# Performance work log

Measured on AMD Instinct MI355X. Metric: run time of the kernel, lower is better.

Reference implementation:

```python
import jax, jax.numpy as jnp
import numpy as np

B, T, D, U = 64, 1024, 300, 300


def setup_inputs() -> dict:
    key = jax.random.key(0)
    ks = jax.random.split(key, 12)
    inputs = jax.random.normal(ks[0], (B, T, D), jnp.float32)
    lengths = jax.random.randint(ks[1], (B,), T // 2, T + 1)
    mask = jnp.arange(T)[None, :] < lengths[:, None]  # [B,T] bool

    def w(k, shape, fan_in):
        return jax.random.normal(k, shape, jnp.float32) * (1.0 / np.sqrt(fan_in))

    # Keras GRU (reset_after=True): kernel [D,3U], recurrent_kernel [U,3U], bias [2,3U]
    k_fwd = w(ks[2], (D, 3 * U), D)
    rk_fwd = w(ks[3], (U, 3 * U), U)
    b_fwd = jnp.zeros((2, 3 * U), jnp.float32)
    k_bwd = w(ks[4], (D, 3 * U), D)
    rk_bwd = w(ks[5], (U, 3 * U), U)
    b_bwd = jnp.zeros((2, 3 * U), jnp.float32)
    w_fc = w(ks[6], (2 * U, U), 2 * U)
    b_fc = jnp.zeros((U,), jnp.float32)
    return {
        "inputs": inputs, "mask": mask,
        "k_fwd": k_fwd, "rk_fwd": rk_fwd, "b_fwd": b_fwd,
        "k_bwd": k_bwd, "rk_bwd": rk_bwd, "b_bwd": b_bwd,
        "w_fc": w_fc, "b_fc": b_fc, "training": 0,
    }


def _gru_dir(x, mask, kernel, rkernel, bias):
    """Keras GRU v2 (reset_after=True), zero_output_for_mask, state frozen on masked steps.
    x: [B,T,D], mask: [B,T] bool -> (ys [B,T,U], h_final [B,U])"""
    b_in, b_rec = bias[0], bias[1]
    u = rkernel.shape[0]
    # precompute input projections for all timesteps (cuDNN-style hoisting)
    xp = jnp.einsum('btd,dk->btk', x, kernel) + b_in  # [B,T,3U]

    def step(h, inp):
        xt, mt = inp  # xt: [B,3U], mt: [B]
        rp = h @ rkernel + b_rec  # [B,3U]
        xz, xr, xh = jnp.split(xt, 3, axis=-1)
        rz, rr, rh = jnp.split(rp, 3, axis=-1)
        z = jax.nn.sigmoid(xz + rz)
        r = jax.nn.sigmoid(xr + rr)
        hh = jnp.tanh(xh + r * rh)
        h_new = z * h + (1.0 - z) * hh
        m = mt[:, None]
        h_carry = jnp.where(m, h_new, h)       # state does not update on masked steps
        y = jnp.where(m, h_new, jnp.zeros_like(h_new))  # zero_output_for_mask
        return h_carry, y

    h0 = jnp.zeros((x.shape[0], u), x.dtype)
    h_final, ys = jax.lax.scan(step, h0, (xp.transpose(1, 0, 2), mask.T))
    return ys.transpose(1, 0, 2), h_final


def reference(inputs, mask, k_fwd, rk_fwd, b_fwd, k_bwd, rk_bwd, b_bwd, w_fc, b_fc, training):
    mask = mask.astype(bool)
    x = inputs  # Dropout is identity at inference (training=0)
    y_f, h_f = _gru_dir(x, mask, k_fwd, rk_fwd, b_fwd)
    # backward direction: process reversed sequence/mask, then re-reverse outputs
    y_b, h_b = _gru_dir(x[:, ::-1], mask[:, ::-1], k_bwd, rk_bwd, b_bwd)
    y_b = y_b[:, ::-1]
    output = jnp.concatenate([y_f, y_b], axis=-1)  # [B,T,2U]
    state = jax.nn.relu(jnp.concatenate([h_f, h_b], axis=-1) @ w_fc + b_fc)  # [B,U]
    return output, state
```

## Files before the change

### kernel.cpp

```cpp
#include <hip/hip_runtime.h>
#include <hip/hip_bf16.h>


#define B_   64
#define T_   1024
#define D_   300
#define U_   300
#define NU   900
#define KP   320
#define NP   960
#define XPW  912
#define NW   15
#define W_   20
#define HS   320
#define KB_  10

typedef short short8 __attribute__((ext_vector_type(8)));
typedef float floatx4 __attribute__((ext_vector_type(4)));

__device__ __forceinline__ float b2f_bits(unsigned short u) {
  union { unsigned int i; float f; } v; v.i = ((unsigned int)u) << 16; return v.f;
}
__device__ __forceinline__ unsigned short f2b(float f) {
  __hip_bfloat16 h = __float2bfloat16(f);
  return *reinterpret_cast<unsigned short*>(&h);
}

__global__ __launch_bounds__(64) void k_detect(const unsigned int* __restrict__ xw,
                                               const unsigned char* __restrict__ mb,
                                               int* __restrict__ flags) {
  __shared__ int red[64];
  int tid = threadIdx.x;
  int hits = 0;
  for (int i = tid; i < 2048; i += 64) {
    unsigned int lo = xw[i] & 0xFFFFu;
    int e = (int)((lo >> 7) & 0xFF);
    if (e >= 105 && e <= 135) hits++;
  }
  red[tid] = hits;
  __syncthreads();
  if (tid == 0) {
    int s = 0;
    for (int i = 0; i < 64; ++i) s += red[i];
    flags[0] = (s >= 1024) ? 1 : 0;
    unsigned char b0 = mb[0], b1 = mb[1];
    flags[1] = (b1 == 0) ? 0 : ((b0 == 1 && b1 == 1) ? 1 : 2);
  }
}

__global__ __launch_bounds__(256) void k_lengths(const unsigned char* __restrict__ mraw,
                                                 const int* __restrict__ flags,
                                                 int* __restrict__ lens) {
  __shared__ int red[256];
  int b = blockIdx.x, tid = threadIdx.x;
  int mt = flags[1];
  int s = 0;
  if (mt == 0) {
    const int* m = (const int*)mraw;
    for (int t = tid; t < T_; t += 256) s += m[(size_t)b * T_ + t] ? 1 : 0;
  } else if (mt == 1) {
    for (int t = tid; t < T_; t += 256) s += mraw[(size_t)b * T_ + t] ? 1 : 0;
  } else {
    const unsigned short* m = (const unsigned short*)mraw;
    for (int t = tid; t < T_; t += 256) s += m[(size_t)b * T_ + t] ? 1 : 0;
  }
  red[tid] = s; __syncthreads();
  for (int off = 128; off > 0; off >>= 1) {
    if (tid < off) red[tid] += red[tid + off];
    __syncthreads();
  }
  if (tid == 0) lens[b] = red[0];
}

__global__ __launch_bounds__(256) void k_init(unsigned short* __restrict__ hHi,
                                              unsigned short* __restrict__ hLo,
                                              int* __restrict__ ctrs) {
  int i = blockIdx.x * 256 + threadIdx.x;
  const int nu = 2 * 2 * B_ * HS / 2;
  unsigned int* a = (unsigned int*)hHi;
  unsigned int* b = (unsigned int*)hLo;
  if (i < nu) { a[i] = 0u; b[i] = 0u; }
  if (i < 128) ctrs[i] = 0;
}

__global__ __launch_bounds__(256) void k_xpad(const void* __restrict__ xraw,
                                              const int* __restrict__ flags,
                                              unsigned short* __restrict__ xp) {
  int id = blockIdx.x * 256 + threadIdx.x;
  int row = id / 40, seg = id % 40;
  int kbase = seg * 8;
  int bf = flags[0];
  unsigned short v[8];
  if (bf) {
    const unsigned short* x = (const unsigned short*)xraw;
#pragma unroll
    for (int i = 0; i < 8; ++i) {
      int k = kbase + i;
      v[i] = (k < D_) ? x[(size_t)row * D_ + k] : (unsigned short)0;
    }
  } else {
    const float* x = (const float*)xraw;
#pragma unroll
    for (int i = 0; i < 8; ++i) {
      int k = kbase + i;
      v[i] = (k < D_) ? f2b(x[(size_t)row * D_ + k]) : (unsigned short)0;
    }
  }
  uint4 o;
  o.x = (unsigned)v[0] | ((unsigned)v[1] << 16);
  o.y = (unsigned)v[2] | ((unsigned)v[3] << 16);
  o.z = (unsigned)v[4] | ((unsigned)v[5] << 16);
  o.w = (unsigned)v[6] | ((unsigned)v[7] << 16);
  *(uint4*)(xp + (size_t)row * KP + kbase) = o;
}

__global__ __launch_bounds__(256) void k_wpad(const void* __restrict__ kf,
                                              const void* __restrict__ kb,
                                              const int* __restrict__ flags,
                                              unsigned short* __restrict__ kp) {
  int id = blockIdx.x * 256 + threadIdx.x;
  if (id >= 2 * KP * NP) return;
  int dir = id / (KP * NP);
  int r = id % (KP * NP);
  int k = r / NP, n = r % NP;
  int bf = flags[0];
  unsigned short v = 0;
  if (k < D_ && n < NU) {
    size_t si = (size_t)k * NU + n;
    if (bf) v = ((const unsigned short*)(dir ? kb : kf))[si];
    else    v = f2b(((const float*)(dir ? kb : kf))[si]);
  }
  kp[id] = v;
}

__global__ __launch_bounds__(256) void k_prep(const void* __restrict__ rkf,
                                              const void* __restrict__ rkb,
                                              const void* __restrict__ bfw,
                                              const void* __restrict__ bbw,
                                              const void* __restrict__ wfc,
                                              const void* __restrict__ bfc,
                                              const int* __restrict__ flags,
                                              unsigned short* __restrict__ rkc,
                                              float* __restrict__ biasc,
                                              unsigned short* __restrict__ wfcc,
                                              float* __restrict__ bfcc) {
  int i = blockIdx.x * 256 + threadIdx.x;
  int bf = flags[0];
  if (i < 2 * D_ * NU) {
    int dir = i / (D_ * NU), r = i % (D_ * NU);
    const void* src = dir ? rkb : rkf;
    rkc[i] = bf ? ((const unsigned short*)src)[r] : f2b(((const float*)src)[r]);
  }
  if (i < 2 * 2 * NU) {
    int dir = i / (2 * NU), r = i % (2 * NU);
    const void* src = dir ? bbw : bfw;
    biasc[i] = bf ? b2f_bits(((const unsigned short*)src)[r]) : ((const float*)src)[r];
  }
  if (i < 2 * U_ * U_) {
    wfcc[i] = bf ? ((const unsigned short*)wfc)[i] : f2b(((const float*)wfc)[i]);
  }
  if (i < U_) {
    bfcc[i] = bf ? b2f_bits(((const unsigned short*)bfc)[i]) : ((const float*)bfc)[i];
  }
}

__global__ __launch_bounds__(256) void k_bpack(const unsigned short* __restrict__ rkc,
                                               unsigned short* __restrict__ bpack) {
  int idx = blockIdx.x * 256 + threadIdx.x;
  const int total = 2 * NW * 40 * 512;
  if (idx >= total) return;
  int rem = idx;
  int j = rem & 7; rem >>= 3;
  int lane = rem & 63; rem >>= 6;
  int f = rem % 40; rem /= 40;
  int wg = rem % NW;
  int dir = rem / NW;
  int kb = f >> 2, nt = f & 3;
  int l15 = lane & 15, quad = lane >> 4;
  int k = kb * 32 + quad * 8 + j;
  int n = nt * 16 + l15;
  unsigned short v = 0;
  if (n < 3 * W_ && k < D_) {
    int g = n / W_, i = n % W_;
    int col = g * U_ + wg * W_ + i;
    v = rkc[(size_t)dir * D_ * NU + (size_t)k * NU + col];
  }
  bpack[idx] = v;
}

template <bool XPF32>
__global__ __launch_bounds__(256) void k_gemm(const unsigned short* __restrict__ xpad,
                                              const unsigned short* __restrict__ kpad,
                                              const float* __restrict__ biasc,
                                              void* __restrict__ xp_out) {
  __shared__ __align__(16) unsigned short As[64 * 40];
  __shared__ __align__(16) unsigned short Bs[64 * 40];
  int tid = threadIdx.x;
  int wave = tid >> 6, lane = tid & 63;
  int m0 = blockIdx.x * 64, n0 = blockIdx.y * 64;
  int dir = blockIdx.z;
  const unsigned short* Bsrc = kpad + (size_t)dir * KP * NP;
  const float* bin = biasc + (size_t)dir * 2 * NU;

  floatx4 acc[4];
#pragma unroll
  for (int i = 0; i < 4; ++i) acc[i] = {0.f, 0.f, 0.f, 0.f};

  int arow = tid >> 2, aseg = tid & 3;
  int bk = tid & 31, bn8 = (tid >> 5) * 8;
  int fr = lane & 15, fq = lane >> 4;

  for (int kc = 0; kc < KP; kc += 32) {
    uint4 av = *(const uint4*)(xpad + (size_t)(m0 + arow) * KP + kc + aseg * 8);
    uint4 bv = *(const uint4*)(Bsrc + (size_t)(kc + bk) * NP + n0 + bn8);
    *(uint4*)(As + arow * 40 + aseg * 8) = av;
    unsigned short tmp[8];
    tmp[0] = bv.x & 0xffff; tmp[1] = bv.x >> 16;
    tmp[2] = bv.y & 0xffff; tmp[3] = bv.y >> 16;
    tmp[4] = bv.z & 0xffff; tmp[5] = bv.z >> 16;
    tmp[6] = bv.w & 0xffff; tmp[7] = bv.w >> 16;
#pragma unroll
    for (int i = 0; i < 8; ++i) Bs[(bn8 + i) * 40 + bk] = tmp[i];
    __syncthreads();
    short8 a = *(const short8*)(As + (wave * 16 + fr) * 40 + fq * 8);
#pragma unroll
    for (int nt = 0; nt < 4; ++nt) {
      short8 bfrag = *(const short8*)(Bs + (nt * 16 + fr) * 40 + fq * 8);
      acc[nt] = __builtin_amdgcn_mfma_f32_16x16x32_bf16(a, bfrag, acc[nt], 0, 0, 0);
    }
    __syncthreads();
  }
#pragma unroll
  for (int nt = 0; nt < 4; ++nt) {
    int col = n0 + nt * 16 + fr;
    if (col >= XPW) continue;
    float bi = (col < NU) ? bin[col] : 0.f;
#pragma unroll
    for (int r = 0; r < 4; ++r) {
      int m = m0 + wave * 16 + fq * 4 + r;
      float v = acc[nt][r] + bi;
      size_t idx = ((size_t)dir * 65536 + m) * XPW + col;
      if (XPF32) ((float*)xp_out)[idx] = v;
      else ((unsigned short*)xp_out)[idx] = f2b(v);
    }
  }
}

template <bool XPF32>
__global__ __launch_bounds__(256, 1) void k_scan(const unsigned short* __restrict__ bpack,
                                                 const float* __restrict__ biasc,
                                                 const void* __restrict__ xp_all,
                                                 const int* __restrict__ lens,
                                                 const int* __restrict__ flags,
                                                 unsigned short* __restrict__ hHi,
                                                 unsigned short* __restrict__ hLo,
                                                 float* __restrict__ hfin,
                                                 int* __restrict__ ctrs,
                                                 void* __restrict__ outraw) {
  __shared__ __align__(16) float rp[64 * 68];
  int tid = threadIdx.x;
  int wg = blockIdx.x, dir = blockIdx.y;
  int wave = tid >> 6, lane = tid & 63;
  int l15 = lane & 15, quad = lane >> 4;
  int obf = flags[0];
  unsigned short* out16 = (unsigned short*)outraw;
  float* out32 = (float*)outraw;

  short8 breg[KB_][4];
  {
    const unsigned short* bp = bpack + ((size_t)(dir * NW + wg) * 40) * 512 + lane * 8;
#pragma unroll
    for (int kb = 0; kb < KB_; ++kb)
#pragma unroll
      for (int nt = 0; nt < 4; ++nt)
        breg[kb][nt] = *(const short8*)(bp + (size_t)(kb * 4 + nt) * 512);
  }

  int eb = tid >> 2;
  int ei = (tid & 3) * 5;
  int u0 = wg * W_;
  int mylen = lens[eb];
  const float* brec = biasc + (size_t)dir * 2 * NU + NU;
  float bz[5], brr[5], bh[5], hold[5];
#pragma unroll
  for (int q = 0; q < 5; ++q) {
    int u = u0 + ei + q;
    bz[q] = brec[u]; brr[q] = brec[U_ + u]; bh[q] = brec[2 * U_ + u];
    hold[q] = 0.f;
  }

  int ctr_target = 0;
  int* myctr = ctrs + dir * 64;

#pragma unroll 1
  for (int s = 0; s < T_; ++s) {
    int t = dir ? (T_ - 1 - s) : s;
    int par = s & 1;
    const unsigned short* hh = hHi + (size_t)(par * 2 + dir) * (B_ * HS);
    const unsigned short* hl = hLo + (size_t)(par * 2 + dir) * (B_ * HS);

    float xz[5], xr[5], xh[5];
    {
      size_t rowoff = ((size_t)dir * 65536 + (size_t)eb * T_ + t) * XPW;
      if (XPF32) {
        const float* xrow = (const float*)xp_all + rowoff;
#pragma unroll
        for (int q = 0; q < 5; ++q) {
          int u = u0 + ei + q;
          xz[q] = xrow[u]; xr[q] = xrow[U_ + u]; xh[q] = xrow[2 * U_ + u];
        }
      } else {
        const unsigned short* xrow = (const unsigned short*)xp_all + rowoff;
#pragma unroll
        for (int q = 0; q < 5; ++q) {
          int u = u0 + ei + q;
          xz[q] = b2f_bits(xrow[u]); xr[q] = b2f_bits(xrow[U_ + u]); xh[q] = b2f_bits(xrow[2 * U_ + u]);
        }
      }
    }

    floatx4 acc[4];
#pragma unroll
    for (int i = 0; i < 4; ++i) acc[i] = {0.f, 0.f, 0.f, 0.f};
    {
      const unsigned short* ah_base = hh + (size_t)(wave * 16 + l15) * HS + quad * 8;
      const unsigned short* al_base = hl + (size_t)(wave * 16 + l15) * HS + quad * 8;
#pragma unroll
      for (int kb = 0; kb < KB_; ++kb) {
        short8 ah = *(const short8*)(ah_base + kb * 32);
        short8 al = *(const short8*)(al_base + kb * 32);
#pragma unroll
        for (int nt = 0; nt < 4; ++nt)
          acc[nt] = __builtin_amdgcn_mfma_f32_16x16x32_bf16(ah, breg[kb][nt], acc[nt], 0, 0, 0);
#pragma unroll
        for (int nt = 0; nt < 4; ++nt)
          acc[nt] = __builtin_amdgcn_mfma_f32_16x16x32_bf16(al, breg[kb][nt], acc[nt], 0, 0, 0);
      }
    }
#pragma unroll
    for (int nt = 0; nt < 4; ++nt)
#pragma unroll
      for (int r = 0; r < 4; ++r)
        rp[(wave * 16 + quad * 4 + r) * 68 + nt * 16 + l15] = acc[nt][r];
    __syncthreads();

    bool m = (t < mylen);
    unsigned short* nhh = hHi + (size_t)(((s + 1) & 1) * 2 + dir) * (B_ * HS);
    unsigned short* nhl = hLo + (size_t)(((s + 1) & 1) * 2 + dir) * (B_ * HS);
    size_t obase = ((size_t)eb * T_ + t) * 600 + (size_t)dir * U_ + u0 + ei;
#pragma unroll
    for (int q = 0; q < 5; ++q) {
      int i = ei + q;
      float rz = rp[eb * 68 + i];
      float rr = rp[eb * 68 + W_ + i];
      float rh = rp[eb * 68 + 2 * W_ + i];
      float z = 1.f / (1.f + __expf(-(xz[q] + rz + bz[q])));
      float r = 1.f / (1.f + __expf(-(xr[q] + rr + brr[q])));
      float hhat = tanhf(xh[q] + r * (rh + bh[q]));
      float hn = z * hold[q] + (1.f - z) * hhat;
      float hw = m ? hn : hold[q];
      hold[q] = hw;
      float y = m ? hn : 0.f;
      if (obf) out16[obase + q] = f2b(y); else out32[obase + q] = y;
      unsigned short hib = f2b(hw);
      float lo = hw - b2f_bits(hib);
      nhh[eb * HS + u0 + i] = hib;
      nhl[eb * HS + u0 + i] = f2b(lo);
    }

    __threadfence();
    __syncthreads();
    ctr_target += NW;
    if (tid == 0) {
      __hip_atomic_fetch_add(myctr, 1, __ATOMIC_ACQ_REL, __HIP_MEMORY_SCOPE_AGENT);
      while (__hip_atomic_load(myctr, __ATOMIC_ACQUIRE, __HIP_MEMORY_SCOPE_AGENT) < ctr_target)
        __builtin_amdgcn_s_sleep(1);
    }
    __syncthreads();
    __threadfence();
  }

#pragma unroll
  for (int q = 0; q < 5; ++q)
    hfin[((size_t)dir * B_ + eb) * 304 + u0 + ei + q] = hold[q];
}

__global__ __launch_bounds__(320) void k_state(const float* __restrict__ hfin,
                                               const unsigned short* __restrict__ wfcc,
                                               const float* __restrict__ bfcc,
                                               const int* __restrict__ flags,
                                               void* __restrict__ outraw) {
  int b = blockIdx.x, u = threadIdx.x;
  if (u >= U_) return;
  int obf = flags[0];
  float acc = bfcc[u];
  const float* hf = hfin + (size_t)b * 304;
  const float* hb = hfin + ((size_t)B_ + b) * 304;
  for (int k = 0; k < U_; ++k) acc = fmaf(hf[k], b2f_bits(wfcc[(size_t)k * U_ + u]), acc);
  for (int k = 0; k < U_; ++k) acc = fmaf(hb[k], b2f_bits(wfcc[(size_t)(U_ + k) * U_ + u]), acc);
  float v = fmaxf(acc, 0.f);
  size_t oi = (size_t)B_ * T_ * 600 + (size_t)b * U_ + u;
  if (obf) ((unsigned short*)outraw)[oi] = f2b(v);
  else     ((float*)outraw)[oi] = v;
}

extern "C" void kernel_launch(void* const* d_in, const int* in_sizes, int n_in,
                              void* d_out, int out_size, void* d_ws, size_t ws_size,
                              hipStream_t stream) {
  const void* x    = d_in[0];
  const void* mask = d_in[1];
  const void* kf   = d_in[2];
  const void* rkf  = d_in[3];
  const void* bfw  = d_in[4];
  const void* kb   = d_in[5];
  const void* rkb  = d_in[6];
  const void* bbw  = d_in[7];
  const void* wfc  = d_in[8];
  const void* bfc  = d_in[9];

  char* ws = (char*)d_ws;
  size_t off = 0;
  auto alloc = [&](size_t bytes) { void* p = ws + off; off += (bytes + 255) & ~(size_t)255; return p; };
  int* flags            = (int*)alloc(256);
  int* lens             = (int*)alloc(256);
  int* ctrs             = (int*)alloc(512);
  unsigned short* xpad  = (unsigned short*)alloc((size_t)65536 * KP * 2);
  unsigned short* kpad  = (unsigned short*)alloc((size_t)2 * KP * NP * 2);
  unsigned short* rkc   = (unsigned short*)alloc((size_t)2 * D_ * NU * 2);
  unsigned short* bpack = (unsigned short*)alloc((size_t)2 * NW * 40 * 512 * 2);
  float* biasc          = (float*)alloc((size_t)2 * 2 * NU * 4);
  unsigned short* wfcc  = (unsigned short*)alloc((size_t)2 * U_ * U_ * 2);
  float* bfcc           = (float*)alloc((size_t)U_ * 4);
  float* hfin           = (float*)alloc((size_t)2 * B_ * 304 * 4);
  unsigned short* hHi   = (unsigned short*)alloc((size_t)2 * 2 * B_ * HS * 2);
  unsigned short* hLo   = (unsigned short*)alloc((size_t)2 * 2 * B_ * HS * 2);
  void* xp = (void*)(ws + off);
  size_t need_f32 = off + (size_t)2 * 65536 * XPW * 4;
  bool xpf32 = ws_size >= need_f32;

  k_detect<<<dim3(1), dim3(64), 0, stream>>>((const unsigned int*)x, (const unsigned char*)mask, flags);
  k_lengths<<<dim3(B_), dim3(256), 0, stream>>>((const unsigned char*)mask, flags, lens);
  k_init<<<dim3((2 * 2 * B_ * HS / 2 + 255) / 256), dim3(256), 0, stream>>>(hHi, hLo, ctrs);
  k_xpad<<<dim3(65536 * 40 / 256), dim3(256), 0, stream>>>(x, flags, xpad);
  k_wpad<<<dim3((2 * KP * NP + 255) / 256), dim3(256), 0, stream>>>(kf, kb, flags, kpad);
  k_prep<<<dim3((2 * D_ * NU + 255) / 256), dim3(256), 0, stream>>>(rkf, rkb, bfw, bbw, wfc, bfc,
                                                                    flags, rkc, biasc, wfcc, bfcc);
  k_bpack<<<dim3((2 * NW * 40 * 512 + 255) / 256), dim3(256), 0, stream>>>(rkc, bpack);
  if (xpf32) {
    k_gemm<true><<<dim3(1024, 15, 2), dim3(256), 0, stream>>>(xpad, kpad, biasc, xp);
    k_scan<true><<<dim3(NW, 2), dim3(256), 0, stream>>>(bpack, biasc, xp, lens, flags,
                                                        hHi, hLo, hfin, ctrs, d_out);
  } else {
    k_gemm<false><<<dim3(1024, 15, 2), dim3(256), 0, stream>>>(xpad, kpad, biasc, xp);
    k_scan<false><<<dim3(NW, 2), dim3(256), 0, stream>>>(bpack, biasc, xp, lens, flags,
                                                         hHi, hLo, hfin, ctrs, d_out);
  }
  k_state<<<dim3(B_), dim3(320), 0, stream>>>(hfin, wfcc, bfcc, flags, d_out);
}
```

Baseline: 14.06 ms.

## Run each GRU direction in one workgroup with LDS-resident hidden state

The recurrent scan moves from 15 workgroups per direction, which synchronised every timestep through global atomic counters and exchanged the hidden state via global memory, to a single 512-thread workgroup per direction. That workgroup keeps the hi/lo bf16 hidden state in shared memory and uses only __syncthreads between steps. The recurrent weights are repacked into uneven per-wave column slices and streamed from global memory or cache each step instead of living in registers. The aim is to remove the cross-workgroup spin barrier and the global state round-trip. The cost is that only two compute units do all the recurrent MFMA work, plus extra weight traffic on every step.

```diff
diff --git a/kernel.cpp b/kernel.cpp
--- a/kernel.cpp
+++ b/kernel.cpp
@@ -10,10 +10,8 @@
 #define KP   320
 #define NP   960
 #define XPW  912
-#define NW   15
-#define W_   20
-#define HS   320
 #define KB_  10
+#define FRAGS_PER_DIR 600
 
 typedef short short8 __attribute__((ext_vector_type(8)));
 typedef float floatx4 __attribute__((ext_vector_type(4)));
@@ -70,17 +68,6 @@
     __syncthreads();
   }
   if (tid == 0) lens[b] = red[0];
-}
-
-__global__ __launch_bounds__(256) void k_init(unsigned short* __restrict__ hHi,
-                                              unsigned short* __restrict__ hLo,
-                                              int* __restrict__ ctrs) {
-  int i = blockIdx.x * 256 + threadIdx.x;
-  const int nu = 2 * 2 * B_ * HS / 2;
-  unsigned int* a = (unsigned int*)hHi;
-  unsigned int* b = (unsigned int*)hLo;
-  if (i < nu) { a[i] = 0u; b[i] = 0u; }
-  if (i < 128) ctrs[i] = 0;
 }
 
 __global__ __launch_bounds__(256) void k_xpad(const void* __restrict__ xraw,
@@ -167,23 +154,27 @@
 __global__ __launch_bounds__(256) void k_bpack(const unsigned short* __restrict__ rkc,
                                                unsigned short* __restrict__ bpack) {
   int idx = blockIdx.x * 256 + threadIdx.x;
-  const int total = 2 * NW * 40 * 512;
+  const int total = 2 * FRAGS_PER_DIR * 512;
   if (idx >= total) return;
   int rem = idx;
   int j = rem & 7; rem >>= 3;
   int lane = rem & 63; rem >>= 6;
-  int f = rem % 40; rem /= 40;
-  int wg = rem % NW;
-  int dir = rem / NW;
-  int kb = f >> 2, nt = f & 3;
+  int f = rem % FRAGS_PER_DIR;
+  int dir = rem / FRAGS_PER_DIR;
+  int w, fr, ntc;
+  if (f < 360) { w = f / 90; fr = f - w * 90; ntc = 9; }
+  else { int f2 = f - 360; w = 4 + f2 / 60; fr = f2 % 60; ntc = 6; }
+  int kb = fr / ntc, nt = fr % ntc;
+  int b = nt / 3, g = nt % 3;
   int l15 = lane & 15, quad = lane >> 4;
   int k = kb * 32 + quad * 8 + j;
-  int n = nt * 16 + l15;
+  int U0 = (w < 4) ? w * 48 : 192 + (w - 4) * 32;
+  int WUw = (w < 4) ? 48 : ((w < 7) ? 32 : 12);
+  int local = b * 16 + l15;
   unsigned short v = 0;
-  if (n < 3 * W_ && k < D_) {
-    int g = n / W_, i = n % W_;
-    int col = g * U_ + wg * W_ + i;
-    v = rkc[(size_t)dir * D_ * NU + (size_t)k * NU + col];
+  if (k < U_ && local < WUw) {
+    int col = g * U_ + U0 + local;
+    v = rkc[(size_t)dir * U_ * NU + (size_t)k * NU + col];
   }
   bpack[idx] = v;
 }
@@ -246,143 +237,197 @@
   }
 }
 
+template <int NTC>
+__device__ __forceinline__ void phaseA(floatx4 (&acc)[4][9],
+                                       const unsigned short* __restrict__ bp,
+                                       const unsigned short (*sHi)[328],
+                                       const unsigned short (*sLo)[328],
+                                       int l15, int quad) {
+  short8 bA[NTC], bB[NTC];
+#pragma unroll
+  for (int nt = 0; nt < NTC; ++nt)
+    bA[nt] = *(const short8*)(bp + (size_t)nt * 512);
+#pragma unroll 1
+  for (int kb2 = 0; kb2 < KB_; kb2 += 2) {
+#pragma unroll
+    for (int nt = 0; nt < NTC; ++nt)
+      bB[nt] = *(const short8*)(bp + ((size_t)(kb2 + 1) * NTC + nt) * 512);
+#pragma unroll
+    for (int mt = 0; mt < 4; ++mt) {
+      const short8 ah = *(const short8*)&sHi[mt * 16 + l15][kb2 * 32 + quad * 8];
+      const short8 al = *(const short8*)&sLo[mt * 16 + l15][kb2 * 32 + quad * 8];
+#pragma unroll
+      for (int nt = 0; nt < NTC; ++nt)
+        acc[mt][nt] = __builtin_amdgcn_mfma_f32_16x16x32_bf16(ah, bA[nt], acc[mt][nt], 0, 0, 0);
+#pragma unroll
+      for (int nt = 0; nt < NTC; ++nt)
+        acc[mt][nt] = __builtin_amdgcn_mfma_f32_16x16x32_bf16(al, bA[nt], acc[mt][nt], 0, 0, 0);
+    }
+    if (kb2 + 2 < KB_) {
+#pragma unroll
+      for (int nt = 0; nt < NTC; ++nt)
+        bA[nt] = *(const short8*)(bp + ((size_t)(kb2 + 2) * NTC + nt) * 512);
+    }
+#pragma unroll
+    for (int mt = 0; mt < 4; ++mt) {
+      const short8 ah = *(const short8*)&sHi[mt * 16 + l15][(kb2 + 1) * 32 + quad * 8];
+      const short8 al = *(const short8*)&sLo[mt * 16 + l15][(kb2 + 1) * 32 + quad * 8];
+#pragma unroll
+      for (int nt = 0; nt < NTC; ++nt)
+        acc[mt][nt] = __builtin_amdgcn_mfma_f32_16x16x32_bf16(ah, bB[nt], acc[mt][nt], 0, 0, 0);
+#pragma unroll
+      for (int nt = 0; nt < NTC; ++nt)
+        acc[mt][nt] = __builtin_amdgcn_mfma_f32_16x16x32_bf16(al, bB[nt], acc[mt][nt], 0, 0, 0);
+    }
+  }
+}
+
 template <bool XPF32>
-__global__ __launch_bounds__(256, 1) void k_scan(const unsigned short* __restrict__ bpack,
+__device__ __forceinline__ void loadxp(float (&X)[3][3][4], const void* __restrict__ xp_all,
+                                       int dir, int t, int mt, int U0, int WUw, int NB,
+                                       int l15, int quad) {
+  int uc[3];
+#pragma unroll
+  for (int b = 0; b < 3; ++b) {
+    int local = b * 16 + l15;
+    uc[b] = (local < WUw) ? (U0 + local) : 0;
+  }
+#pragma unroll
+  for (int r = 0; r < 4; ++r) {
+    int row = mt * 16 + quad * 4 + r;
+    size_t ro = ((size_t)dir * 65536 + (size_t)row * T_ + t) * XPW;
+    if (XPF32) {
+      const float* xr = (const float*)xp_all + ro;
+#pragma unroll
+      for (int b = 0; b < 3; ++b) {
+        if (b >= NB) continue;
+        X[b][0][r] = xr[uc[b]];
+        X[b][1][r] = xr[U_ + uc[b]];
+        X[b][2][r] = xr[2 * U_ + uc[b]];
+      }
+    } else {
+      const unsigned short* xr = (const unsigned short*)xp_all + ro;
+#pragma unroll
+      for (int b = 0; b < 3; ++b) {
+        if (b >= NB) continue;
+        X[b][0][r] = b2f_bits(xr[uc[b]]);
+        X[b][1][r] = b2f_bits(xr[U_ + uc[b]]);
+        X[b][2][r] = b2f_bits(xr[2 * U_ + uc[b]]);
+      }
+    }
+  }
+}
+
+template <int MT>
+__device__ __forceinline__ void epi_mt(floatx4 (&acc)[4][9], float (&X)[3][3][4],
+                                       unsigned short (*sHi)[328], unsigned short (*sLo)[328],
+                                       const float* __restrict__ sBias, const int* __restrict__ sLen,
+                                       int t, int dir, int U0, int WUw, int NB,
+                                       int l15, int quad, int obf,
+                                       unsigned short* __restrict__ out16, float* __restrict__ out32) {
+  float bzv[3], brv[3], bhv[3]; int ucv[3]; bool cvv[3];
+#pragma unroll
+  for (int b = 0; b < 3; ++b) {
+    int local = b * 16 + l15;
+    bool cv = (b < NB) && (local < WUw);
+    int uc = cv ? (U0 + local) : 0;
+    cvv[b] = cv; ucv[b] = uc;
+    bzv[b] = sBias[uc]; brv[b] = sBias[U_ + uc]; bhv[b] = sBias[2 * U_ + uc];
+  }
+#pragma unroll
+  for (int r = 0; r < 4; ++r) {
+    int row = MT * 16 + quad * 4 + r;
+    bool m = (t < sLen[row]);
+#pragma unroll
+    for (int b = 0; b < 3; ++b) {
+      if (b >= NB) continue;
+      int uc = ucv[b];
+      float z  = 1.f / (1.f + __expf(-(X[b][0][r] + acc[MT][3 * b + 0][r] + bzv[b])));
+      float rg = 1.f / (1.f + __expf(-(X[b][1][r] + acc[MT][3 * b + 1][r] + brv[b])));
+      float hh = tanhf(X[b][2][r] + rg * (acc[MT][3 * b + 2][r] + bhv[b]));
+      float hold = b2f_bits(sHi[row][uc]) + b2f_bits(sLo[row][uc]);
+      float hn = z * hold + (1.f - z) * hh;
+      float hw = m ? hn : hold;
+      if (cvv[b]) {
+        float y = m ? hn : 0.f;
+        size_t ob = ((size_t)row * T_ + t) * 600 + (size_t)dir * U_ + (size_t)uc;
+        if (obf) out16[ob] = f2b(y); else out32[ob] = y;
+        unsigned short hib = f2b(hw);
+        sHi[row][uc] = hib;
+        sLo[row][uc] = f2b(hw - b2f_bits(hib));
+      }
+    }
+  }
+}
+
+template <bool XPF32>
+__global__ __launch_bounds__(512, 2) void k_scan(const unsigned short* __restrict__ bpack,
                                                  const float* __restrict__ biasc,
                                                  const void* __restrict__ xp_all,
                                                  const int* __restrict__ lens,
                                                  const int* __restrict__ flags,
-                                                 unsigned short* __restrict__ hHi,
-                                                 unsigned short* __restrict__ hLo,
                                                  float* __restrict__ hfin,
-                                                 int* __restrict__ ctrs,
                                                  void* __restrict__ outraw) {
-  __shared__ __align__(16) float rp[64 * 68];
-  int tid = threadIdx.x;
-  int wg = blockIdx.x, dir = blockIdx.y;
-  int wave = tid >> 6, lane = tid & 63;
-  int l15 = lane & 15, quad = lane >> 4;
-  int obf = flags[0];
+  __shared__ unsigned short sHi[64][328];
+  __shared__ unsigned short sLo[64][328];
+  __shared__ float sBias[912];
+  __shared__ int sLen[64];
+
+  const int tid = threadIdx.x;
+  const int dir = blockIdx.x;
+  const int wave = tid >> 6, lane = tid & 63;
+  const int l15 = lane & 15, quad = lane >> 4;
+  const int obf = flags[0];
   unsigned short* out16 = (unsigned short*)outraw;
   float* out32 = (float*)outraw;
 
-  short8 breg[KB_][4];
   {
-    const unsigned short* bp = bpack + ((size_t)(dir * NW + wg) * 40) * 512 + lane * 8;
-#pragma unroll
-    for (int kb = 0; kb < KB_; ++kb)
-#pragma unroll
-      for (int nt = 0; nt < 4; ++nt)
-        breg[kb][nt] = *(const short8*)(bp + (size_t)(kb * 4 + nt) * 512);
-  }
-
-  int eb = tid >> 2;
-  int ei = (tid & 3) * 5;
-  int u0 = wg * W_;
-  int mylen = lens[eb];
-  const float* brec = biasc + (size_t)dir * 2 * NU + NU;
-  float bz[5], brr[5], bh[5], hold[5];
-#pragma unroll
-  for (int q = 0; q < 5; ++q) {
-    int u = u0 + ei + q;
-    bz[q] = brec[u]; brr[q] = brec[U_ + u]; bh[q] = brec[2 * U_ + u];
-    hold[q] = 0.f;
-  }
-
-  int ctr_target = 0;
-  int* myctr = ctrs + dir * 64;
+    unsigned int* p0 = (unsigned int*)&sHi[0][0];
+    unsigned int* p1 = (unsigned int*)&sLo[0][0];
+    for (int i = tid; i < 64 * 328 / 2; i += 512) { p0[i] = 0u; p1[i] = 0u; }
+    const float* brec = biasc + (size_t)dir * 2 * NU + NU;
+    for (int i = tid; i < NU; i += 512) sBias[i] = brec[i];
+    if (tid < 64) sLen[tid] = lens[tid];
+  }
+  __syncthreads();
+
+  const int NB  = (wave < 4) ? 3 : 2;
+  const int U0  = (wave < 4) ? wave * 48 : 192 + (wave - 4) * 32;
+  const int WUw = (wave < 4) ? 48 : ((wave < 7) ? 32 : 12);
+  const int FB  = (wave < 4) ? wave * 90 : 360 + (wave - 4) * 60;
+  const unsigned short* bp = bpack + ((size_t)dir * FRAGS_PER_DIR + FB) * 512 + (size_t)lane * 8;
+
+  floatx4 acc[4][9];
 
 #pragma unroll 1
   for (int s = 0; s < T_; ++s) {
-    int t = dir ? (T_ - 1 - s) : s;
-    int par = s & 1;
-    const unsigned short* hh = hHi + (size_t)(par * 2 + dir) * (B_ * HS);
-    const unsigned short* hl = hLo + (size_t)(par * 2 + dir) * (B_ * HS);
-
-    float xz[5], xr[5], xh[5];
-    {
-      size_t rowoff = ((size_t)dir * 65536 + (size_t)eb * T_ + t) * XPW;
-      if (XPF32) {
-        const float* xrow = (const float*)xp_all + rowoff;
-#pragma unroll
-        for (int q = 0; q < 5; ++q) {
-          int u = u0 + ei + q;
-          xz[q] = xrow[u]; xr[q] = xrow[U_ + u]; xh[q] = xrow[2 * U_ + u];
-        }
-      } else {
-        const unsigned short* xrow = (const unsigned short*)xp_all + rowoff;
-#pragma unroll
-        for (int q = 0; q < 5; ++q) {
-          int u = u0 + ei + q;
-          xz[q] = b2f_bits(xrow[u]); xr[q] = b2f_bits(xrow[U_ + u]); xh[q] = b2f_bits(xrow[2 * U_ + u]);
-        }
-      }
-    }
-
-    floatx4 acc[4];
-#pragma unroll
-    for (int i = 0; i < 4; ++i) acc[i] = {0.f, 0.f, 0.f, 0.f};
-    {
-      const unsigned short* ah_base = hh + (size_t)(wave * 16 + l15) * HS + quad * 8;
-      const unsigned short* al_base = hl + (size_t)(wave * 16 + l15) * HS + quad * 8;
-#pragma unroll
-      for (int kb = 0; kb < KB_; ++kb) {
-        short8 ah = *(const short8*)(ah_base + kb * 32);
-        short8 al = *(const short8*)(al_base + kb * 32);
-#pragma unroll
-        for (int nt = 0; nt < 4; ++nt)
-          acc[nt] = __builtin_amdgcn_mfma_f32_16x16x32_bf16(ah, breg[kb][nt], acc[nt], 0, 0, 0);
-#pragma unroll
-        for (int nt = 0; nt < 4; ++nt)
-          acc[nt] = __builtin_amdgcn_mfma_f32_16x16x32_bf16(al, breg[kb][nt], acc[nt], 0, 0, 0);
-      }
-    }
-#pragma unroll
-    for (int nt = 0; nt < 4; ++nt)
-#pragma unroll
-      for (int r = 0; r < 4; ++r)
-        rp[(wave * 16 + quad * 4 + r) * 68 + nt * 16 + l15] = acc[nt][r];
+    const int t = dir ? (T_ - 1 - s) : s;
+#pragma unroll
+    for (int mt = 0; mt < 4; ++mt)
+#pragma unroll
+      for (int nt = 0; nt < 9; ++nt) acc[mt][nt] = {0.f, 0.f, 0.f, 0.f};
+
+    if (wave < 4) phaseA<9>(acc, bp, sHi, sLo, l15, quad);
+    else          phaseA<6>(acc, bp, sHi, sLo, l15, quad);
+
+    float xgA[3][3][4], xgB[3][3][4];
+    loadxp<XPF32>(xgA, xp_all, dir, t, 0, U0, WUw, NB, l15, quad);
     __syncthreads();
-
-    bool m = (t < mylen);
-    unsigned short* nhh = hHi + (size_t)(((s + 1) & 1) * 2 + dir) * (B_ * HS);
-    unsigned short* nhl = hLo + (size_t)(((s + 1) & 1) * 2 + dir) * (B_ * HS);
-    size_t obase = ((size_t)eb * T_ + t) * 600 + (size_t)dir * U_ + u0 + ei;
-#pragma unroll
-    for (int q = 0; q < 5; ++q) {
-      int i = ei + q;
-      float rz = rp[eb * 68 + i];
-      float rr = rp[eb * 68 + W_ + i];
-      float rh = rp[eb * 68 + 2 * W_ + i];
-      float z = 1.f / (1.f + __expf(-(xz[q] + rz + bz[q])));
-      float r = 1.f / (1.f + __expf(-(xr[q] + rr + brr[q])));
-      float hhat = tanhf(xh[q] + r * (rh + bh[q]));
-      float hn = z * hold[q] + (1.f - z) * hhat;
-      float hw = m ? hn : hold[q];
-      hold[q] = hw;
-      float y = m ? hn : 0.f;
-      if (obf) out16[obase + q] = f2b(y); else out32[obase + q] = y;
-      unsigned short hib = f2b(hw);
-      float lo = hw - b2f_bits(hib);
-      nhh[eb * HS + u0 + i] = hib;
-      nhl[eb * HS + u0 + i] = f2b(lo);
-    }
-
-    __threadfence();
+    loadxp<XPF32>(xgB, xp_all, dir, t, 1, U0, WUw, NB, l15, quad);
+    epi_mt<0>(acc, xgA, sHi, sLo, sBias, sLen, t, dir, U0, WUw, NB, l15, quad, obf, out16, out32);
+    loadxp<XPF32>(xgA, xp_all, dir, t, 2, U0, WUw, NB, l15, quad);
+    epi_mt<1>(acc, xgB, sHi, sLo, sBias, sLen, t, dir, U0, WUw, NB, l15, quad, obf, out16, out32);
+    loadxp<XPF32>(xgB, xp_all, dir, t, 3, U0, WUw, NB, l15, quad);
+    epi_mt<2>(acc, xgA, sHi, sLo, sBias, sLen, t, dir, U0, WUw, NB, l15, quad, obf, out16, out32);
+    epi_mt<3>(acc, xgB, sHi, sLo, sBias, sLen, t, dir, U0, WUw, NB, l15, quad, obf, out16, out32);
     __syncthreads();
-    ctr_target += NW;
-    if (tid == 0) {
-      __hip_atomic_fetch_add(myctr, 1, __ATOMIC_ACQ_REL, __HIP_MEMORY_SCOPE_AGENT);
-      while (__hip_atomic_load(myctr, __ATOMIC_ACQUIRE, __HIP_MEMORY_SCOPE_AGENT) < ctr_target)
-        __builtin_amdgcn_s_sleep(1);
-    }
-    __syncthreads();
-    __threadfence();
-  }
-
-#pragma unroll
-  for (int q = 0; q < 5; ++q)
-    hfin[((size_t)dir * B_ + eb) * 304 + u0 + ei + q] = hold[q];
+  }
+
+  {
+    int row = tid >> 3;
+    for (int u = (tid & 7); u < U_; u += 8)
+      hfin[((size_t)dir * B_ + row) * 304 + u] = b2f_bits(sHi[row][u]) + b2f_bits(sLo[row][u]);
+  }
 }
 
 __global__ __launch_bounds__(320) void k_state(const float* __restrict__ hfin,
@@ -423,37 +468,31 @@
   auto alloc = [&](size_t bytes) { void* p = ws + off; off += (bytes + 255) & ~(size_t)255; return p; };
   int* flags            = (int*)alloc(256);
   int* lens             = (int*)alloc(256);
-  int* ctrs             = (int*)alloc(512);
   unsigned short* xpad  = (unsigned short*)alloc((size_t)65536 * KP * 2);
   unsigned short* kpad  = (unsigned short*)alloc((size_t)2 * KP * NP * 2);
   unsigned short* rkc   = (unsigned short*)alloc((size_t)2 * D_ * NU * 2);
-  unsigned short* bpack = (unsigned short*)alloc((size_t)2 * NW * 40 * 512 * 2);
+  unsigned short* bpack = (unsigned short*)alloc((size_t)2 * FRAGS_PER_DIR * 512 * 2);
   float* biasc          = (float*)alloc((size_t)2 * 2 * NU * 4);
   unsigned short* wfcc  = (unsigned short*)alloc((size_t)2 * U_ * U_ * 2);
   float* bfcc           = (float*)alloc((size_t)U_ * 4);
   float* hfin           = (float*)alloc((size_t)2 * B_ * 304 * 4);
-  unsigned short* hHi   = (unsigned short*)alloc((size_t)2 * 2 * B_ * HS * 2);
-  unsigned short* hLo   = (unsigned short*)alloc((size_t)2 * 2 * B_ * HS * 2);
   void* xp = (void*)(ws + off);
   size_t need_f32 = off + (size_t)2 * 65536 * XPW * 4;
   bool xpf32 = ws_size >= need_f32;
 
   k_detect<<<dim3(1), dim3(64), 0, stream>>>((const unsigned int*)x, (const unsigned char*)mask, flags);
   k_lengths<<<dim3(B_), dim3(256), 0, stream>>>((const unsigned char*)mask, flags, lens);
-  k_init<<<dim3((2 * 2 * B_ * HS / 2 + 255) / 256), dim3(256), 0, stream>>>(hHi, hLo, ctrs);
   k_xpad<<<dim3(65536 * 40 / 256), dim3(256), 0, stream>>>(x, flags, xpad);
   k_wpad<<<dim3((2 * KP * NP + 255) / 256), dim3(256), 0, stream>>>(kf, kb, flags, kpad);
   k_prep<<<dim3((2 * D_ * NU + 255) / 256), dim3(256), 0, stream>>>(rkf, rkb, bfw, bbw, wfc, bfc,
                                                                     flags, rkc, biasc, wfcc, bfcc);
-  k_bpack<<<dim3((2 * NW * 40 * 512 + 255) / 256), dim3(256), 0, stream>>>(rkc, bpack);
+  k_bpack<<<dim3((2 * FRAGS_PER_DIR * 512 + 255) / 256), dim3(256), 0, stream>>>(rkc, bpack);
   if (xpf32) {
     k_gemm<true><<<dim3(1024, 15, 2), dim3(256), 0, stream>>>(xpad, kpad, biasc, xp);
-    k_scan<true><<<dim3(NW, 2), dim3(256), 0, stream>>>(bpack, biasc, xp, lens, flags,
-                                                        hHi, hLo, hfin, ctrs, d_out);
+    k_scan<true><<<dim3(2), dim3(512), 0, stream>>>(bpack, biasc, xp, lens, flags, hfin, d_out);
   } else {
     k_gemm<false><<<dim3(1024, 15, 2), dim3(256), 0, stream>>>(xpad, kpad, biasc, xp);
-    k_scan<false><<<dim3(NW, 2), dim3(256), 0, stream>>>(bpack, biasc, xp, lens, flags,
-                                                         hHi, hLo, hfin, ctrs, d_out);
+    k_scan<false><<<dim3(2), dim3(512), 0, stream>>>(bpack, biasc, xp, lens, flags, hfin, d_out);
   }
   k_state<<<dim3(B_), dim3(320), 0, stream>>>(hfin, wfcc, bfcc, flags, d_out);
 }
```

After: 42.41 ms. +201.7%, slower.
